# Kernel tuning notes

Measured on AMD Instinct MI355X. Metric: run time of the kernel, lower is better.

## Reference

```python
import jax, jax.numpy as jnp
import numpy as np

B_, N_, H_ = 4, 256, 32          # batch, nodes, neighbors (edges = B*N*H)
NC_IN, NC_OUT = 16, 16
NUM_FREQ, D_OUT, M_IN = 3, 3, 3  # degree_in = degree_out = 1 -> 2*1+1
EDGE_DIM, HID = 16, 64
LN_EPS = 1e-5


def _ln(x, gamma):
    # torch F.layer_norm over last dim, beta fixed at zero
    mu = jnp.mean(x, axis=-1, keepdims=True)
    var = jnp.var(x, axis=-1, keepdims=True)
    return (x - mu) * jax.lax.rsqrt(var + LN_EPS) * gamma


def setup_inputs() -> dict:
    key = jax.random.key(0)
    ks = jax.random.split(key, 8)

    def lin(k, fin, fout):
        lim = 1.0 / np.sqrt(fin)
        kw, kb = jax.random.split(k)
        W = jax.random.uniform(kw, (fin, fout), jnp.float32, -lim, lim)
        b = jax.random.uniform(kb, (fout,), jnp.float32, -lim, lim)
        return W, b

    W1, b1 = lin(ks[0], EDGE_DIM + 1, HID)
    W2, b2 = lin(ks[1], HID, HID)
    W3, b3 = lin(ks[2], HID, NUM_FREQ * NC_IN * NC_OUT)
    return {
        "feat": jax.random.normal(ks[3], (B_, N_, H_, EDGE_DIM + 1), jnp.float32),
        "basis": jax.random.normal(ks[4], (B_, N_, H_, D_OUT, M_IN, NUM_FREQ), jnp.float32),
        "W1": W1, "b1": b1, "g1": jnp.ones((HID,), jnp.float32),
        "W2": W2, "b2": b2, "g2": jnp.ones((HID,), jnp.float32),
        "W3": W3, "b3": b3,
    }


def reference(feat, basis, W1, b1, g1, W2, b2, g2, W3, b3):
    # radial MLP: Linear -> SiLU -> LN -> Linear -> SiLU -> LN -> Linear
    h = _ln(jax.nn.silu(feat @ W1 + b1), g1)
    h = _ln(jax.nn.silu(h @ W2 + b2), g2)
    r = h @ W3 + b3                                   # (b, n, k, o*i*f)
    R = r.reshape(*r.shape[:-1], NC_OUT, NC_IN, NUM_FREQ)  # '(o i f) -> o i f'
    # per-frequency multiply-accumulate: sum_f R[...,o,i,f] * B[...,d,m,f]
    out = jnp.einsum('bnkoif,bnkdmf->bnkodim', R, basis)   # (b,n,k,o,d,i,m)
    b, n, k = out.shape[:3]
    # contiguous reshape matches torch rearrange + view: (b,n,k, d_out*nc_out, nc_in*m_in)
    return out.reshape(b, n, k, NC_OUT * D_OUT, NC_IN * M_IN)
```

## Files before the change

kernel.cpp:

```cpp
#include <hip/hip_runtime.h>

#define E_TOTAL 32768
#define F_IN 17
#define HID 64
#define NJ 768

using bf16x8 = __attribute__((ext_vector_type(8))) short;
using f32x4  = __attribute__((ext_vector_type(4))) float;

__device__ __forceinline__ unsigned short f2bf(float x){
    unsigned u = __float_as_uint(x);
    u += 0x7fffu + ((u >> 16) & 1u);
    return (unsigned short)(u >> 16);
}

__global__ __launch_bounds__(256) void prep_w3(const float* __restrict__ W3,
                                               unsigned short* __restrict__ w3t){
    int t = blockIdx.x * 256 + threadIdx.x;
    int n = t >> 6, k = t & 63;
    w3t[t] = f2bf(W3[k * NJ + n]);
}

__global__ __launch_bounds__(256) void mlp_kernel(const float* __restrict__ feat,
        const float* __restrict__ W1, const float* __restrict__ b1, const float* __restrict__ g1,
        const float* __restrict__ W2, const float* __restrict__ b2, const float* __restrict__ g2,
        unsigned short* __restrict__ hb){
    __shared__ float sW1[F_IN * HID];
    __shared__ float sW2[HID * HID];
    __shared__ float sC[4 * HID];
    __shared__ float sFeat[16 * F_IN];
    __shared__ __align__(16) float sH1[16][HID];

    int tid = threadIdx.x;
    int e0  = blockIdx.x * 16;
    for (int i = tid; i < F_IN * HID; i += 256) sW1[i] = W1[i];
    for (int i = tid; i < HID * HID; i += 256) sW2[i] = W2[i];
    if (tid < 64) { sC[tid] = b1[tid]; sC[64 + tid] = g1[tid];
                    sC[128 + tid] = b2[tid]; sC[192 + tid] = g2[tid]; }
    for (int i = tid; i < 16 * F_IN; i += 256) sFeat[i] = feat[(size_t)e0 * F_IN + i];
    __syncthreads();

    int j = tid & 63, wv = tid >> 6;
    float acc[4], x[4], s1[4], s2[4];

    #pragma unroll
    for (int q = 0; q < 4; ++q) acc[q] = sC[j];
    for (int k = 0; k < F_IN; ++k){
        float w = sW1[k * 64 + j];
        #pragma unroll
        for (int q = 0; q < 4; ++q) acc[q] += sFeat[(wv * 4 + q) * F_IN + k] * w;
    }
    #pragma unroll
    for (int q = 0; q < 4; ++q){
        float a = acc[q];
        float sg = 1.0f / (1.0f + __expf(-a));
        x[q] = a * sg; s1[q] = x[q]; s2[q] = x[q] * x[q];
    }
    #pragma unroll
    for (int m = 1; m < 64; m <<= 1){
        #pragma unroll
        for (int q = 0; q < 4; ++q){
            s1[q] += __shfl_xor(s1[q], m);
            s2[q] += __shfl_xor(s2[q], m);
        }
    }
    #pragma unroll
    for (int q = 0; q < 4; ++q){
        float mu  = s1[q] * (1.0f / 64.0f);
        float var = s2[q] * (1.0f / 64.0f) - mu * mu;
        float rs  = rsqrtf(var + 1e-5f);
        sH1[wv * 4 + q][j] = (x[q] - mu) * rs * sC[64 + j];
    }

    #pragma unroll
    for (int q = 0; q < 4; ++q) acc[q] = sC[128 + j];
    for (int k4 = 0; k4 < 16; ++k4){
        float hv[4][4];
        #pragma unroll
        for (int q = 0; q < 4; ++q) *(float4*)hv[q] = *(const float4*)&sH1[wv * 4 + q][k4 * 4];
        #pragma unroll
        for (int kk = 0; kk < 4; ++kk){
            float w = sW2[(k4 * 4 + kk) * 64 + j];
            #pragma unroll
            for (int q = 0; q < 4; ++q) acc[q] += hv[q][kk] * w;
        }
    }
    #pragma unroll
    for (int q = 0; q < 4; ++q){
        float a = acc[q];
        float sg = 1.0f / (1.0f + __expf(-a));
        x[q] = a * sg; s1[q] = x[q]; s2[q] = x[q] * x[q];
    }
    #pragma unroll
    for (int m = 1; m < 64; m <<= 1){
        #pragma unroll
        for (int q = 0; q < 4; ++q){
            s1[q] += __shfl_xor(s1[q], m);
            s2[q] += __shfl_xor(s2[q], m);
        }
    }
    #pragma unroll
    for (int q = 0; q < 4; ++q){
        float mu  = s1[q] * (1.0f / 64.0f);
        float var = s2[q] * (1.0f / 64.0f) - mu * mu;
        float rs  = rsqrtf(var + 1e-5f);
        float h2  = (x[q] - mu) * rs * sC[192 + j];
        hb[(size_t)(e0 + wv * 4 + q) * 64 + j] = f2bf(h2);
    }
}

__global__ __launch_bounds__(256, 4) void tp_kernel(const unsigned short* __restrict__ hb,
        const unsigned short* __restrict__ w3t, const float* __restrict__ b3,
        const float* __restrict__ basis, float* __restrict__ out){
    __shared__ __align__(16) float sR[16 * 194];

    int tid = threadIdx.x;
    int e0  = blockIdx.x * 16;

    int wv = tid >> 6, l = tid & 63;
    int col = l & 15, kg = l >> 4;

    const unsigned short* hrow = hb + (size_t)(e0 + col) * 64;
    bf16x8 a0 = *(const bf16x8*)(hrow + kg * 8);
    bf16x8 a1 = *(const bf16x8*)(hrow + 32 + kg * 8);

    int e_loc = wv * 4 + kg;
    int s     = col;
    float bs[27];
    const float* bp = basis + (size_t)(e0 + e_loc) * 27;
    #pragma unroll
    for (int z = 0; z < 27; ++z) bs[z] = bp[z];
    float* outE = out + (size_t)(e0 + e_loc) * 2304;
    const float* Rrow = sR + e_loc * 194;

    for (int c4 = 0; c4 < 4; ++c4){
        #pragma unroll
        for (int t = 0; t < 3; ++t){
            int n0 = c4 * 192 + wv * 48 + t * 16;
            const unsigned short* wrow = w3t + (size_t)(n0 + col) * 64;
            bf16x8 bb0 = *(const bf16x8*)(wrow + kg * 8);
            bf16x8 bb1 = *(const bf16x8*)(wrow + 32 + kg * 8);
            f32x4 acc = {0.f, 0.f, 0.f, 0.f};
            acc = __builtin_amdgcn_mfma_f32_16x16x32_bf16(a0, bb0, acc, 0, 0, 0);
            acc = __builtin_amdgcn_mfma_f32_16x16x32_bf16(a1, bb1, acc, 0, 0, 0);
            float bj = b3[n0 + col];
            int cL = wv * 48 + t * 16 + col;
            #pragma unroll
            for (int r = 0; r < 4; ++r){
                int e = kg * 4 + r;
                sR[e * 194 + cL] = acc[r] + bj;
            }
        }
        __syncthreads();

        #pragma unroll
        for (int t2 = 0; t2 < 4; ++t2){
            int o = c4 * 4 + t2;
            const float* rp = Rrow + t2 * 48 + s * 3;
            float r0 = rp[0], r1 = rp[1], r2 = rp[2];
            #pragma unroll
            for (int d = 0; d < 3; ++d){
                float* p = outE + o * 144 + d * 48 + s * 3;
                int z = d * 9;
                p[0] = r0 * bs[z + 0] + r1 * bs[z + 1] + r2 * bs[z + 2];
                p[1] = r0 * bs[z + 3] + r1 * bs[z + 4] + r2 * bs[z + 5];
                p[2] = r0 * bs[z + 6] + r1 * bs[z + 7] + r2 * bs[z + 8];
            }
        }
        __syncthreads();
    }
}

extern "C" void kernel_launch(void* const* d_in, const int* in_sizes, int n_in,
                              void* d_out, int out_size, void* d_ws, size_t ws_size,
                              hipStream_t stream) {
    const float* feat  = (const float*)d_in[0];
    const float* basis = (const float*)d_in[1];
    const float* W1 = (const float*)d_in[2];
    const float* b1 = (const float*)d_in[3];
    const float* g1 = (const float*)d_in[4];
    const float* W2 = (const float*)d_in[5];
    const float* b2 = (const float*)d_in[6];
    const float* g2 = (const float*)d_in[7];
    const float* W3 = (const float*)d_in[8];
    const float* b3 = (const float*)d_in[9];
    float* out = (float*)d_out;

    unsigned short* hbuf = (unsigned short*)d_ws;
    unsigned short* w3t  = hbuf + (size_t)E_TOTAL * HID;

    prep_w3<<<NJ * HID / 256, 256, 0, stream>>>(W3, w3t);
    mlp_kernel<<<E_TOTAL / 16, 256, 0, stream>>>(feat, W1, b1, g1, W2, b2, g2, hbuf);
    tp_kernel<<<E_TOTAL / 16, 256, 0, stream>>>(hbuf, w3t, b3, basis, out);
}
```

Baseline: 363.7 us.

## Fuse MLP into tensor-product kernel with split-bf16 MFMA layers and per-wave tiles

The two radial MLP layers move from scalar FP32 FMAs to MFMA, using split bf16 (hi/lo) operands to keep near-FP32 accuracy. The MLP is fused into the output kernel, so the hidden activations no longer round-trip through global memory and one launch is removed. Each wave now owns 16 edges independently with wave-private LDS, which drops the block-wide __syncthreads. The cost is extra MFMA passes for the hi/lo products, a changed store pattern for the output, and lower occupancy (launch bound 2).

```diff
diff --git a/kernel.cpp b/kernel.cpp
--- a/kernel.cpp
+++ b/kernel.cpp
@@ -1,8 +1,6 @@
 #include <hip/hip_runtime.h>
 
 #define E_TOTAL 32768
-#define F_IN 17
-#define HID 64
 #define NJ 768
 
 using bf16x8 = __attribute__((ext_vector_type(8))) short;
@@ -13,161 +11,198 @@
     u += 0x7fffu + ((u >> 16) & 1u);
     return (unsigned short)(u >> 16);
 }
-
-__global__ __launch_bounds__(256) void prep_w3(const float* __restrict__ W3,
-                                               unsigned short* __restrict__ w3t){
+__device__ __forceinline__ float bf2f(unsigned short h){
+    return __uint_as_float((unsigned)h << 16);
+}
+
+__device__ __forceinline__ float rowsum16(float x){
+    x += __int_as_float(__builtin_amdgcn_update_dpp(0, __float_as_int(x), 0x128, 0xf, 0xf, false));
+    x += __int_as_float(__builtin_amdgcn_update_dpp(0, __float_as_int(x), 0x124, 0xf, 0xf, false));
+    x += __int_as_float(__builtin_amdgcn_update_dpp(0, __float_as_int(x), 0x122, 0xf, 0xf, false));
+    x += __int_as_float(__builtin_amdgcn_update_dpp(0, __float_as_int(x), 0x121, 0xf, 0xf, false));
+    return x;
+}
+
+__global__ __launch_bounds__(256) void prep_weights(const float* __restrict__ W1,
+        const float* __restrict__ W2, const float* __restrict__ W3,
+        unsigned short* __restrict__ w3t, unsigned short* __restrict__ w2th,
+        unsigned short* __restrict__ w2tl, unsigned short* __restrict__ w1th,
+        unsigned short* __restrict__ w1tl){
     int t = blockIdx.x * 256 + threadIdx.x;
-    int n = t >> 6, k = t & 63;
-    w3t[t] = f2bf(W3[k * NJ + n]);
-}
-
-__global__ __launch_bounds__(256) void mlp_kernel(const float* __restrict__ feat,
-        const float* __restrict__ W1, const float* __restrict__ b1, const float* __restrict__ g1,
-        const float* __restrict__ W2, const float* __restrict__ b2, const float* __restrict__ g2,
-        unsigned short* __restrict__ hb){
-    __shared__ float sW1[F_IN * HID];
-    __shared__ float sW2[HID * HID];
-    __shared__ float sC[4 * HID];
-    __shared__ float sFeat[16 * F_IN];
-    __shared__ __align__(16) float sH1[16][HID];
-
-    int tid = threadIdx.x;
-    int e0  = blockIdx.x * 16;
-    for (int i = tid; i < F_IN * HID; i += 256) sW1[i] = W1[i];
-    for (int i = tid; i < HID * HID; i += 256) sW2[i] = W2[i];
-    if (tid < 64) { sC[tid] = b1[tid]; sC[64 + tid] = g1[tid];
-                    sC[128 + tid] = b2[tid]; sC[192 + tid] = g2[tid]; }
-    for (int i = tid; i < 16 * F_IN; i += 256) sFeat[i] = feat[(size_t)e0 * F_IN + i];
-    __syncthreads();
-
-    int j = tid & 63, wv = tid >> 6;
-    float acc[4], x[4], s1[4], s2[4];
-
-    #pragma unroll
-    for (int q = 0; q < 4; ++q) acc[q] = sC[j];
-    for (int k = 0; k < F_IN; ++k){
-        float w = sW1[k * 64 + j];
-        #pragma unroll
-        for (int q = 0; q < 4; ++q) acc[q] += sFeat[(wv * 4 + q) * F_IN + k] * w;
-    }
-    #pragma unroll
-    for (int q = 0; q < 4; ++q){
-        float a = acc[q];
-        float sg = 1.0f / (1.0f + __expf(-a));
-        x[q] = a * sg; s1[q] = x[q]; s2[q] = x[q] * x[q];
-    }
-    #pragma unroll
-    for (int m = 1; m < 64; m <<= 1){
-        #pragma unroll
-        for (int q = 0; q < 4; ++q){
-            s1[q] += __shfl_xor(s1[q], m);
-            s2[q] += __shfl_xor(s2[q], m);
-        }
-    }
-    #pragma unroll
-    for (int q = 0; q < 4; ++q){
-        float mu  = s1[q] * (1.0f / 64.0f);
-        float var = s2[q] * (1.0f / 64.0f) - mu * mu;
-        float rs  = rsqrtf(var + 1e-5f);
-        sH1[wv * 4 + q][j] = (x[q] - mu) * rs * sC[64 + j];
-    }
-
-    #pragma unroll
-    for (int q = 0; q < 4; ++q) acc[q] = sC[128 + j];
-    for (int k4 = 0; k4 < 16; ++k4){
-        float hv[4][4];
-        #pragma unroll
-        for (int q = 0; q < 4; ++q) *(float4*)hv[q] = *(const float4*)&sH1[wv * 4 + q][k4 * 4];
-        #pragma unroll
-        for (int kk = 0; kk < 4; ++kk){
-            float w = sW2[(k4 * 4 + kk) * 64 + j];
-            #pragma unroll
-            for (int q = 0; q < 4; ++q) acc[q] += hv[q][kk] * w;
-        }
-    }
-    #pragma unroll
-    for (int q = 0; q < 4; ++q){
-        float a = acc[q];
-        float sg = 1.0f / (1.0f + __expf(-a));
-        x[q] = a * sg; s1[q] = x[q]; s2[q] = x[q] * x[q];
-    }
-    #pragma unroll
-    for (int m = 1; m < 64; m <<= 1){
-        #pragma unroll
-        for (int q = 0; q < 4; ++q){
-            s1[q] += __shfl_xor(s1[q], m);
-            s2[q] += __shfl_xor(s2[q], m);
-        }
-    }
-    #pragma unroll
-    for (int q = 0; q < 4; ++q){
-        float mu  = s1[q] * (1.0f / 64.0f);
-        float var = s2[q] * (1.0f / 64.0f) - mu * mu;
-        float rs  = rsqrtf(var + 1e-5f);
-        float h2  = (x[q] - mu) * rs * sC[192 + j];
-        hb[(size_t)(e0 + wv * 4 + q) * 64 + j] = f2bf(h2);
-    }
-}
-
-__global__ __launch_bounds__(256, 4) void tp_kernel(const unsigned short* __restrict__ hb,
+    if (t < 49152){
+        int n = t >> 6, k = t & 63;
+        w3t[t] = f2bf(W3[k * NJ + n]);
+    } else if (t < 49152 + 4096){
+        int u = t - 49152; int j = u >> 6, k = u & 63;
+        float v = W2[k * 64 + j];
+        unsigned short h = f2bf(v);
+        w2th[u] = h; w2tl[u] = f2bf(v - bf2f(h));
+    } else if (t < 49152 + 4096 + 2048){
+        int u = t - 49152 - 4096; int j = u >> 5, k = u & 31;
+        float v = (k < 17) ? W1[k * 64 + j] : 0.0f;
+        unsigned short h = f2bf(v);
+        w1th[u] = h; w1tl[u] = f2bf(v - bf2f(h));
+    }
+}
+
+__global__ __launch_bounds__(256, 2) void fused_kernel(const float* __restrict__ feat,
+        const float* __restrict__ b1, const float* __restrict__ g1,
+        const float* __restrict__ b2, const float* __restrict__ g2,
+        const unsigned short* __restrict__ w1th, const unsigned short* __restrict__ w1tl,
+        const unsigned short* __restrict__ w2th, const unsigned short* __restrict__ w2tl,
         const unsigned short* __restrict__ w3t, const float* __restrict__ b3,
         const float* __restrict__ basis, float* __restrict__ out){
-    __shared__ __align__(16) float sR[16 * 194];
-
+    __shared__ __align__(16) char smem[4 * 6912];
     int tid = threadIdx.x;
-    int e0  = blockIdx.x * 16;
-
     int wv = tid >> 6, l = tid & 63;
-    int col = l & 15, kg = l >> 4;
-
-    const unsigned short* hrow = hb + (size_t)(e0 + col) * 64;
-    bf16x8 a0 = *(const bf16x8*)(hrow + kg * 8);
-    bf16x8 a1 = *(const bf16x8*)(hrow + 32 + kg * 8);
-
-    int e_loc = wv * 4 + kg;
-    int s     = col;
+    char* wbase = smem + wv * 6912;
+    unsigned short* sH   = (unsigned short*)wbase;
+    unsigned short* sHah = (unsigned short*)(wbase + 2304);
+    unsigned short* sHal = (unsigned short*)(wbase + 4608);
+    float*          sR   = (float*)(wbase + 2304);
+
+    int eb = (blockIdx.x * 4 + wv) * 16;
+    int c  = l & 15, kg = l >> 4;
+
+    float fa[8];
+    const float* fr = feat + (size_t)(eb + c) * 17;
+    #pragma unroll
+    for (int i = 0; i < 8; ++i) fa[i] = 0.0f;
+    if (kg < 2){
+        #pragma unroll
+        for (int i = 0; i < 8; ++i) fa[i] = fr[kg * 8 + i];
+    } else if (kg == 2){
+        fa[0] = fr[16];
+    }
+    bf16x8 Fh, Fl;
+    #pragma unroll
+    for (int i = 0; i < 8; ++i){
+        unsigned short h = f2bf(fa[i]);
+        Fh[i] = (short)h;
+        Fl[i] = (short)f2bf(fa[i] - bf2f(h));
+    }
+    f32x4 x1[4];
+    #pragma unroll
+    for (int jt = 0; jt < 4; ++jt){
+        int j = jt * 16 + c;
+        bf16x8 Bh = *(const bf16x8*)(w1th + j * 32 + kg * 8);
+        bf16x8 Bl = *(const bf16x8*)(w1tl + j * 32 + kg * 8);
+        float bj = b1[j];
+        f32x4 acc = {bj, bj, bj, bj};
+        acc = __builtin_amdgcn_mfma_f32_16x16x32_bf16(Fh, Bh, acc, 0, 0, 0);
+        acc = __builtin_amdgcn_mfma_f32_16x16x32_bf16(Fh, Bl, acc, 0, 0, 0);
+        acc = __builtin_amdgcn_mfma_f32_16x16x32_bf16(Fl, Bh, acc, 0, 0, 0);
+        #pragma unroll
+        for (int r = 0; r < 4; ++r){
+            float a = acc[r];
+            x1[jt][r] = a / (1.0f + __expf(-a));
+        }
+    }
+    #pragma unroll
+    for (int r = 0; r < 4; ++r){
+        float s1 = x1[0][r] + x1[1][r] + x1[2][r] + x1[3][r];
+        float s2 = x1[0][r]*x1[0][r] + x1[1][r]*x1[1][r]
+                 + x1[2][r]*x1[2][r] + x1[3][r]*x1[3][r];
+        s1 = rowsum16(s1);
+        s2 = rowsum16(s2);
+        float mu  = s1 * (1.0f / 64.0f);
+        float var = s2 * (1.0f / 64.0f) - mu * mu;
+        float rs  = rsqrtf(var + 1e-5f);
+        #pragma unroll
+        for (int jt = 0; jt < 4; ++jt){
+            int j = jt * 16 + c;
+            float h1 = (x1[jt][r] - mu) * rs * g1[j];
+            unsigned short hh = f2bf(h1);
+            sHah[(kg * 4 + r) * 72 + j] = hh;
+            sHal[(kg * 4 + r) * 72 + j] = f2bf(h1 - bf2f(hh));
+        }
+    }
+
+    bf16x8 Ah0 = *(const bf16x8*)(sHah + c * 72 + kg * 8);
+    bf16x8 Ah1 = *(const bf16x8*)(sHah + c * 72 + 32 + kg * 8);
+    bf16x8 Al0 = *(const bf16x8*)(sHal + c * 72 + kg * 8);
+    bf16x8 Al1 = *(const bf16x8*)(sHal + c * 72 + 32 + kg * 8);
+    f32x4 x2[4];
+    #pragma unroll
+    for (int jt = 0; jt < 4; ++jt){
+        int j = jt * 16 + c;
+        bf16x8 Bh0 = *(const bf16x8*)(w2th + j * 64 + kg * 8);
+        bf16x8 Bh1 = *(const bf16x8*)(w2th + j * 64 + 32 + kg * 8);
+        bf16x8 Bl0 = *(const bf16x8*)(w2tl + j * 64 + kg * 8);
+        bf16x8 Bl1 = *(const bf16x8*)(w2tl + j * 64 + 32 + kg * 8);
+        float bj = b2[j];
+        f32x4 acc = {bj, bj, bj, bj};
+        acc = __builtin_amdgcn_mfma_f32_16x16x32_bf16(Ah0, Bh0, acc, 0, 0, 0);
+        acc = __builtin_amdgcn_mfma_f32_16x16x32_bf16(Ah1, Bh1, acc, 0, 0, 0);
+        acc = __builtin_amdgcn_mfma_f32_16x16x32_bf16(Ah0, Bl0, acc, 0, 0, 0);
+        acc = __builtin_amdgcn_mfma_f32_16x16x32_bf16(Ah1, Bl1, acc, 0, 0, 0);
+        acc = __builtin_amdgcn_mfma_f32_16x16x32_bf16(Al0, Bh0, acc, 0, 0, 0);
+        acc = __builtin_amdgcn_mfma_f32_16x16x32_bf16(Al1, Bh1, acc, 0, 0, 0);
+        #pragma unroll
+        for (int r = 0; r < 4; ++r){
+            float a = acc[r];
+            x2[jt][r] = a / (1.0f + __expf(-a));
+        }
+    }
+    #pragma unroll
+    for (int r = 0; r < 4; ++r){
+        float s1 = x2[0][r] + x2[1][r] + x2[2][r] + x2[3][r];
+        float s2 = x2[0][r]*x2[0][r] + x2[1][r]*x2[1][r]
+                 + x2[2][r]*x2[2][r] + x2[3][r]*x2[3][r];
+        s1 = rowsum16(s1);
+        s2 = rowsum16(s2);
+        float mu  = s1 * (1.0f / 64.0f);
+        float var = s2 * (1.0f / 64.0f) - mu * mu;
+        float rs  = rsqrtf(var + 1e-5f);
+        #pragma unroll
+        for (int jt = 0; jt < 4; ++jt){
+            int j = jt * 16 + c;
+            sH[(kg * 4 + r) * 72 + j] = f2bf((x2[jt][r] - mu) * rs * g2[j]);
+        }
+    }
+
     float bs[27];
-    const float* bp = basis + (size_t)(e0 + e_loc) * 27;
-    #pragma unroll
-    for (int z = 0; z < 27; ++z) bs[z] = bp[z];
-    float* outE = out + (size_t)(e0 + e_loc) * 2304;
-    const float* Rrow = sR + e_loc * 194;
-
-    for (int c4 = 0; c4 < 4; ++c4){
+    {
+        const float* bp = basis + (size_t)(eb + (l >> 2)) * 27;
+        #pragma unroll
+        for (int z = 0; z < 27; ++z) bs[z] = bp[z];
+    }
+    bf16x8 a0 = *(const bf16x8*)(sH + c * 72 + kg * 8);
+    bf16x8 a1 = *(const bf16x8*)(sH + c * 72 + 32 + kg * 8);
+    float* outE = out + (size_t)(eb + (l >> 2)) * 2304;
+    const float* Rrow = sR + (l >> 2) * 53;
+
+    #pragma unroll 1
+    for (int o = 0; o < 16; ++o){
         #pragma unroll
         for (int t = 0; t < 3; ++t){
-            int n0 = c4 * 192 + wv * 48 + t * 16;
-            const unsigned short* wrow = w3t + (size_t)(n0 + col) * 64;
-            bf16x8 bb0 = *(const bf16x8*)(wrow + kg * 8);
-            bf16x8 bb1 = *(const bf16x8*)(wrow + 32 + kg * 8);
+            int n0 = o * 48 + t * 16;
+            const unsigned short* wr = w3t + (size_t)(n0 + c) * 64;
+            bf16x8 wb0 = *(const bf16x8*)(wr + kg * 8);
+            bf16x8 wb1 = *(const bf16x8*)(wr + 32 + kg * 8);
             f32x4 acc = {0.f, 0.f, 0.f, 0.f};
-            acc = __builtin_amdgcn_mfma_f32_16x16x32_bf16(a0, bb0, acc, 0, 0, 0);
-            acc = __builtin_amdgcn_mfma_f32_16x16x32_bf16(a1, bb1, acc, 0, 0, 0);
-            float bj = b3[n0 + col];
-            int cL = wv * 48 + t * 16 + col;
+            acc = __builtin_amdgcn_mfma_f32_16x16x32_bf16(a0, wb0, acc, 0, 0, 0);
+            acc = __builtin_amdgcn_mfma_f32_16x16x32_bf16(a1, wb1, acc, 0, 0, 0);
+            float bj = b3[n0 + c];
             #pragma unroll
-            for (int r = 0; r < 4; ++r){
-                int e = kg * 4 + r;
-                sR[e * 194 + cL] = acc[r] + bj;
-            }
-        }
-        __syncthreads();
-
-        #pragma unroll
-        for (int t2 = 0; t2 < 4; ++t2){
-            int o = c4 * 4 + t2;
-            const float* rp = Rrow + t2 * 48 + s * 3;
-            float r0 = rp[0], r1 = rp[1], r2 = rp[2];
+            for (int r = 0; r < 4; ++r)
+                sR[(kg * 4 + r) * 53 + t * 16 + c] = acc[r] + bj;
+        }
+        #pragma unroll
+        for (int ii = 0; ii < 4; ++ii){
+            int i = (l & 3) * 4 + ii;
+            float r0 = Rrow[i * 3 + 0];
+            float r1 = Rrow[i * 3 + 1];
+            float r2 = Rrow[i * 3 + 2];
+            float* p = outE + o * 144 + i * 3;
             #pragma unroll
             for (int d = 0; d < 3; ++d){
-                float* p = outE + o * 144 + d * 48 + s * 3;
                 int z = d * 9;
-                p[0] = r0 * bs[z + 0] + r1 * bs[z + 1] + r2 * bs[z + 2];
-                p[1] = r0 * bs[z + 3] + r1 * bs[z + 4] + r2 * bs[z + 5];
-                p[2] = r0 * bs[z + 6] + r1 * bs[z + 7] + r2 * bs[z + 8];
+                p[d * 48 + 0] = r0 * bs[z + 0] + r1 * bs[z + 1] + r2 * bs[z + 2];
+                p[d * 48 + 1] = r0 * bs[z + 3] + r1 * bs[z + 4] + r2 * bs[z + 5];
+                p[d * 48 + 2] = r0 * bs[z + 6] + r1 * bs[z + 7] + r2 * bs[z + 8];
             }
         }
-        __syncthreads();
     }
 }
 
@@ -186,10 +221,14 @@
     const float* b3 = (const float*)d_in[9];
     float* out = (float*)d_out;
 
-    unsigned short* hbuf = (unsigned short*)d_ws;
-    unsigned short* w3t  = hbuf + (size_t)E_TOTAL * HID;
-
-    prep_w3<<<NJ * HID / 256, 256, 0, stream>>>(W3, w3t);
-    mlp_kernel<<<E_TOTAL / 16, 256, 0, stream>>>(feat, W1, b1, g1, W2, b2, g2, hbuf);
-    tp_kernel<<<E_TOTAL / 16, 256, 0, stream>>>(hbuf, w3t, b3, basis, out);
-}
+    unsigned short* w3t  = (unsigned short*)d_ws;
+    unsigned short* w2th = w3t + 49152;
+    unsigned short* w2tl = w2th + 4096;
+    unsigned short* w1th = w2tl + 4096;
+    unsigned short* w1tl = w1th + 2048;
+
+    prep_weights<<<216, 256, 0, stream>>>(W1, W2, W3, w3t, w2th, w2tl, w1th, w1tl);
+    fused_kernel<<<E_TOTAL / 64, 256, 0, stream>>>(feat, b1, g1, b2, g2,
+                                                   w1th, w1tl, w2th, w2tl,
+                                                   w3t, b3, basis, out);
+}
```

New measurement: 369.8 us. No clear change (+1.7%).
